# Kernel tuning notes

Measured on AMD Instinct MI355X. Metric: run time of the kernel, lower is better.

The kernel has to match this reference:

```python
import jax, jax.numpy as jnp
import numpy as np
from jax import lax

B, S, K = 256, 2048, 16
E, KE, NI = 20, 17, 30


def crf_nll(emissions, mask, tags, transitions, start_transitions, end_transitions):
    """Mean negative log-likelihood of a linear-chain CRF (pytorch-crf/bert4torch math)."""
    dt = emissions.dtype
    maskf = mask.astype(dt)
    # ---- numerator: score of gold path ----
    em_tag = jnp.take_along_axis(emissions, tags[..., None], axis=2)[..., 0]  # [B,S]
    trans_step = transitions[tags[:, :-1], tags[:, 1:]]                        # [B,S-1]
    num = start_transitions[tags[:, 0]] + em_tag[:, 0]
    num = num + jnp.sum((trans_step + em_tag[:, 1:]) * maskf[:, 1:], axis=1)
    lengths = jnp.sum(mask.astype(jnp.int32), axis=1)                          # [B]
    last_tags = jnp.take_along_axis(tags, (lengths - 1)[:, None], axis=1)[:, 0]
    num = num + end_transitions[last_tags]
    # ---- denominator: log partition via forward algorithm (scan over time) ----
    alpha0 = start_transitions[None, :] + emissions[:, 0]                      # [B,K]

    def step(alpha, xs):
        em_t, m_t = xs                                                         # [B,K], [B]
        nxt = jax.nn.logsumexp(alpha[:, :, None] + transitions[None] + em_t[:, None, :], axis=1)
        alpha = jnp.where(m_t[:, None], nxt, alpha)
        return alpha, None

    alpha, _ = lax.scan(step, alpha0,
                        (emissions[:, 1:].swapaxes(0, 1), mask[:, 1:].swapaxes(0, 1)))
    logZ = jax.nn.logsumexp(alpha + end_transitions[None, :], axis=1)          # [B]
    return jnp.mean(logZ - num)


def cross_entropy_mean(logits, labels):
    logp = jax.nn.log_softmax(logits, axis=-1)
    nll = -jnp.take_along_axis(logp, labels[:, None], axis=1)[:, 0]
    return jnp.mean(nll)


def cross_entropy_ignore0(logits, labels):
    logp = jax.nn.log_softmax(logits, axis=-1)
    nll = -jnp.take_along_axis(logp, labels[:, None], axis=1)[:, 0]
    valid = (labels != 0).astype(logits.dtype)
    return jnp.sum(nll * valid) / jnp.maximum(jnp.sum(valid), 1.0)


def setup_inputs() -> dict:
    key = jax.random.key(0)
    ks = jax.random.split(key, 10)
    emission_score = jax.random.normal(ks[0], (B, S, K), dtype=jnp.float32)
    lengths = jax.random.randint(ks[1], (B,), S // 2, S + 1)
    attention_mask = jnp.arange(S)[None, :] < lengths[:, None]                 # bool [B,S]
    entity_logit = jax.random.normal(ks[2], (B, E, KE), dtype=jnp.float32)
    intent_logit = jax.random.normal(ks[3], (B, NI), dtype=jnp.float32)
    seq_labels = jax.random.randint(ks[4], (B, S), 0, K)
    entity_labels = jax.random.randint(ks[5], (B, E), 0, KE)
    intent_labels = jax.random.randint(ks[6], (B,), 0, NI)
    transitions = jax.random.normal(ks[7], (K, K), dtype=jnp.float32) * 0.1
    start_transitions = jax.random.normal(ks[8], (K,), dtype=jnp.float32) * 0.1
    end_transitions = jax.random.normal(ks[9], (K,), dtype=jnp.float32) * 0.1
    return {"emission_score": emission_score, "attention_mask": attention_mask,
            "entity_logit": entity_logit, "intent_logit": intent_logit,
            "seq_labels": seq_labels, "entity_labels": entity_labels,
            "intent_labels": intent_labels, "transitions": transitions,
            "start_transitions": start_transitions, "end_transitions": end_transitions}


def reference(emission_score, attention_mask, entity_logit, intent_logit,
              seq_labels, entity_labels, intent_labels,
              transitions, start_transitions, end_transitions):
    loss_i = cross_entropy_mean(intent_logit, intent_labels)
    loss_e1 = crf_nll(emission_score, attention_mask, seq_labels,
                      transitions, start_transitions, end_transitions)
    loss_e2 = cross_entropy_ignore0(entity_logit.reshape(-1, entity_logit.shape[-1]),
                                    entity_labels.reshape(-1))
    loss = (loss_e1 + loss_e2 + loss_i) / 3.0
    return (loss, loss_e1, loss_e2, loss_i)
```

## Files before the change

### kernel.cpp

```cpp
#include <hip/hip_runtime.h>
#include <hip/hip_bf16.h>

constexpr int B  = 256, S = 2048, K = 16;
constexpr int E  = 20, KE = 17, NI = 30;
constexpr int C  = 32;
constexpr int L  = S / C;

typedef float    f4 __attribute__((ext_vector_type(4)));
typedef short    s4 __attribute__((ext_vector_type(4)));
typedef unsigned u2 __attribute__((ext_vector_type(2)));

__device__ inline unsigned pk2_trunc(float a, float b) {
  return __builtin_amdgcn_perm(__float_as_uint(b), __float_as_uint(a),
                               0x07060302u);
}

#if __has_builtin(__builtin_amdgcn_mfma_f32_16x16x16bf16_1k)
__device__ inline f4 mfma16(s4 a, s4 b, f4 c) {
  return __builtin_amdgcn_mfma_f32_16x16x16bf16_1k(a, b, c, 0, 0, 0);
}
#else
__device__ inline f4 mfma16(s4 a, s4 b, f4 c) {
  f4 d;
  asm volatile("s_nop 1\n\t"
               "v_mfma_f32_16x16x16_bf16 %0, %1, %2, %3\n\t"
               "s_nop 7\n\ts_nop 7"
               : "=&v"(d) : "v"(a), "v"(b), "v"(c));
  return d;
}
#endif

__global__ __launch_bounds__(1024, 4) void k_fused(
    const float* __restrict__ em,
    const float* __restrict__ trans,
    const int* __restrict__ tags,
    const int* __restrict__ mask,
    const float* __restrict__ startT,
    const float* __restrict__ endT,
    const float* __restrict__ intent_logit,
    const int* __restrict__ intent_labels,
    const float* __restrict__ entity_logit,
    const int* __restrict__ entity_labels,
    float* __restrict__ rowCrf,
    float* __restrict__ rowInt,
    float* __restrict__ rowE2,
    float* __restrict__ rowCnt) {
  __shared__ float tl[256];
  __shared__ alignas(16) float Ml[C * 256];
  __shared__ int   sigl[C];
  __shared__ float numl[16];
  __shared__ int   lenl[16];

  int tid = threadIdx.x;
  if (tid < 256) tl[tid] = trans[tid];
  __syncthreads();

  int w = tid >> 6, lane = tid & 63;
  int b  = blockIdx.x;
  int cA = w;
  int cB = 31 - w;
  int g = lane >> 4, j0 = lane & 15;

  float et0 = __expf(tl[(4 * g + 0) * 16 + j0]);
  float et1 = __expf(tl[(4 * g + 1) * 16 + j0]);
  float et2 = __expf(tl[(4 * g + 2) * 16 + j0]);
  float et3 = __expf(tl[(4 * g + 3) * 16 + j0]);

  int tloA = 1 + cA * L;
  int tloB = 1 + cB * L;
  int WA = min(L, S - tloA);
  int WB = min(L, S - tloB);
  const int* mrow = mask + b * S;
  bool mvA = (lane < WA) && (mrow[tloA + lane] != 0);
  bool mvB = (lane < WB) && (mrow[tloB + lane] != 0);
  int nA = __popcll(__ballot(mvA));
  int nB = __popcll(__ballot(mvB));

  const int* trow = tags + b * S;
  int ttA = tloA + min(lane, WA - 1);
  int ttB = tloB + min(lane, WB - 1);
  int tacA = trow[ttA], tapA = trow[ttA - 1];
  int tacB = trow[ttB], tapB = trow[ttB - 1];
  float numc = 0.f;
  if (lane < nA)
    numc += tl[tapA * 16 + tacA] + em[((size_t)b * S + ttA) * 16 + tacA];
  if (lane < nB)
    numc += tl[tapB * 16 + tacB] + em[((size_t)b * S + ttB) * 16 + tacB];
#pragma unroll
  for (int o = 1; o < 64; o <<= 1) numc += __shfl_xor(numc, o);

  f4 accA, accB;
  accA.x = accB.x = (4 * g + 0 == j0) ? 1.f : 0.f;
  accA.y = accB.y = (4 * g + 1 == j0) ? 1.f : 0.f;
  accA.z = accB.z = (4 * g + 2 == j0) ? 1.f : 0.f;
  accA.w = accB.w = (4 * g + 3 == j0) ? 1.f : 0.f;
  int sigA = 0, sigB = 0;
  const f4 zero4 = {0.f, 0.f, 0.f, 0.f};

  const float* empA = em + ((size_t)b * S + tloA) * 16 + j0;
  const float* empB = em + ((size_t)b * S + tloB) * 16 + j0;

  float curA[8], nxtA[8], curB[8], nxtB[8];
#pragma unroll
  for (int u = 0; u < 8; ++u) { curA[u] = empA[16 * u]; curB[u] = empB[16 * u]; }

#define STEP_A(u_)                                                      \
  {                                                                     \
    float ee = __expf(curA[u_]);                                        \
    unsigned a01 = pk2_trunc(et0 * ee, et1 * ee);                       \
    unsigned a23 = pk2_trunc(et2 * ee, et3 * ee);                       \
    unsigned b01 = pk2_trunc(accA.x, accA.y);                           \
    unsigned b23 = pk2_trunc(accA.z, accA.w);                           \
    s4 Af = __builtin_bit_cast(s4, (u2){a01, a23});                     \
    s4 Bf = __builtin_bit_cast(s4, (u2){b01, b23});                     \
    accA = mfma16(Af, Bf, zero4);                                       \
  }
#define STEP_B(u_)                                                      \
  {                                                                     \
    float ee = __expf(curB[u_]);                                        \
    unsigned a01 = pk2_trunc(et0 * ee, et1 * ee);                       \
    unsigned a23 = pk2_trunc(et2 * ee, et3 * ee);                       \
    unsigned b01 = pk2_trunc(accB.x, accB.y);                           \
    unsigned b23 = pk2_trunc(accB.z, accB.w);                           \
    s4 Af = __builtin_bit_cast(s4, (u2){a01, a23});                     \
    s4 Bf = __builtin_bit_cast(s4, (u2){b01, b23});                     \
    accB = mfma16(Af, Bf, zero4);                                       \
  }
#define RESCALE_A                                                       \
  {                                                                     \
    unsigned fb = __builtin_amdgcn_readfirstlane(__float_as_uint(accA.x));\
    int e = (int)((fb >> 23) & 0xffu) - 127;                            \
    e = max(min(e, 126), -126);                                         \
    float sc = __uint_as_float((unsigned)(127 - e) << 23);              \
    accA.x *= sc; accA.y *= sc; accA.z *= sc; accA.w *= sc;             \
    sigA += e;                                                          \
  }
#define RESCALE_B                                                       \
  {                                                                     \
    unsigned fb = __builtin_amdgcn_readfirstlane(__float_as_uint(accB.x));\
    int e = (int)((fb >> 23) & 0xffu) - 127;                            \
    e = max(min(e, 126), -126);                                         \
    float sc = __uint_as_float((unsigned)(127 - e) << 23);              \
    accB.x *= sc; accB.y *= sc; accB.z *= sc; accB.w *= sc;             \
    sigB += e;                                                          \
  }

  int s = 0;
  for (; s + 8 <= nB; s += 8) {
#pragma unroll
    for (int u = 0; u < 8; ++u) {
      nxtA[u] = empA[16 * min(s + 8 + u, WA - 1)];
      nxtB[u] = empB[16 * min(s + 8 + u, WB - 1)];
    }
#pragma unroll
    for (int u = 0; u < 8; ++u) { STEP_A(u) STEP_B(u) }
    RESCALE_A RESCALE_B
#pragma unroll
    for (int u = 0; u < 8; ++u) { curA[u] = nxtA[u]; curB[u] = nxtB[u]; }
  }
  if (s < nB) {
    int m = nB - s;
#pragma unroll
    for (int u = 0; u < 8; ++u)
      if (u < m) STEP_B(u)
    RESCALE_B
  }
  for (; s + 8 <= nA; s += 8) {
#pragma unroll
    for (int u = 0; u < 8; ++u) nxtA[u] = empA[16 * min(s + 8 + u, WA - 1)];
#pragma unroll
    for (int u = 0; u < 8; ++u) STEP_A(u)
    RESCALE_A
#pragma unroll
    for (int u = 0; u < 8; ++u) curA[u] = nxtA[u];
  }
  if (s < nA) {
    int m = nA - s;
#pragma unroll
    for (int u = 0; u < 8; ++u)
      if (u < m) STEP_A(u)
    RESCALE_A
  }
#undef STEP_A
#undef STEP_B
#undef RESCALE_A
#undef RESCALE_B

  int base = (j0 >> 2) * 64 + 16 * g + (j0 & 3);
  float* moA = &Ml[cA * 256];
  moA[base + 0]  = accA.x;
  moA[base + 4]  = accA.y;
  moA[base + 8]  = accA.z;
  moA[base + 12] = accA.w;
  float* moB = &Ml[cB * 256];
  moB[base + 0]  = accB.x;
  moB[base + 4]  = accB.y;
  moB[base + 8]  = accB.z;
  moB[base + 12] = accB.w;
  if (lane == 0) {
    sigl[cA] = sigA;
    sigl[cB] = sigB;
    numl[w]  = numc;
    lenl[w]  = nA + nB + (cA == 0 ? 1 : 0);
  }
  __syncthreads();

  if (w == 0) {
    int l = lane, jb = l & 15, ib = l >> 4;

    float numtot = (l < 16) ? numl[l] : 0.f;
    int   lentot = (l < 16) ? lenl[l] : 0;
#pragma unroll
    for (int o = 1; o < 16; o <<= 1) {
      numtot += __shfl_xor(numtot, o);
      lentot += __shfl_xor(lentot, o);
    }

    const float* erow = em + (size_t)b * S * 16;
    float a0 = startT[jb] + erow[jb];
    float m0 = a0;
#pragma unroll
    for (int o = 1; o < 16; o <<= 1) m0 = fmaxf(m0, __shfl_xor(m0, o));
    float v = __expf(a0 - m0);
    float total = m0;
    int tg0 = tags[(size_t)b * S];
    float num0 = __shfl(a0, tg0);

    int sv = (l < C) ? sigl[l] : 0;
    const f4* mptr = (const f4*)Ml;
    f4 p0 = mptr[0 * 64 + l], p1 = mptr[1 * 64 + l];
    f4 p2 = mptr[2 * 64 + l], p3 = mptr[3 * 64 + l];

#define PROC(p_, c_)                                                         \
    {                                                                        \
      float v0 = __shfl(v, 4 * ib + 0), v1 = __shfl(v, 4 * ib + 1);          \
      float v2 = __shfl(v, 4 * ib + 2), v3 = __shfl(v, 4 * ib + 3);          \
      float sacc = v0 * p_.x + v1 * p_.y + v2 * p_.z + v3 * p_.w;            \
      sacc += __shfl_xor(sacc, 16); sacc += __shfl_xor(sacc, 32);            \
      float mx = sacc;                                                       \
      for (int o = 1; o < 16; o <<= 1) mx = fmaxf(mx, __shfl_xor(mx, o));    \
      int e = (int)((__float_as_uint(mx) >> 23) & 0xffu) - 127;              \
      e = max(min(e, 126), -126);                                            \
      float sc = __uint_as_float((unsigned)(127 - e) << 23);                 \
      v = sacc * sc;                                                         \
      total += (float)(__shfl(sv, (c_)) + e) * 0.6931471805599453f;          \
    }

    for (int cc = 0; cc < C; cc += 4) {
      PROC(p0, cc + 0) if (cc + 4 < C) p0 = mptr[(cc + 4) * 64 + l];
      PROC(p1, cc + 1) if (cc + 4 < C) p1 = mptr[(cc + 5) * 64 + l];
      PROC(p2, cc + 2) if (cc + 4 < C) p2 = mptr[(cc + 6) * 64 + l];
      PROC(p3, cc + 3) if (cc + 4 < C) p3 = mptr[(cc + 7) * 64 + l];
    }
#undef PROC

    float term = v * __expf(endT[jb]);
#pragma unroll
    for (int o = 1; o < 16; o <<= 1) term += __shfl_xor(term, o);
    if (l == 0) {
      float logZ = __logf(term) + total;
      float numb = numtot + num0 + endT[tags[(size_t)b * S + lentot - 1]];
      rowCrf[b] = logZ - numb;
    }
  } else if (w == 1) {
    int l = lane;
    const float* row = intent_logit + b * NI;
    float x = (l < NI) ? row[l] : -1e30f;
    float mi = x;
#pragma unroll
    for (int o = 1; o < 64; o <<= 1) mi = fmaxf(mi, __shfl_xor(mi, o));
    float se = (l < NI) ? __expf(x - mi) : 0.f;
#pragma unroll
    for (int o = 1; o < 64; o <<= 1) se += __shfl_xor(se, o);

    float nll2 = 0.f, cnt2 = 0.f;
    if (l < E) {
      const float* er = entity_logit + (size_t)(b * E + l) * KE;
      float me = -1e30f;
      for (int k = 0; k < KE; ++k) me = fmaxf(me, er[k]);
      float ss = 0.f;
      for (int k = 0; k < KE; ++k) ss += __expf(er[k] - me);
      int lb = entity_labels[b * E + l];
      if (lb != 0) { nll2 = -(er[lb] - me - __logf(ss)); cnt2 = 1.f; }
    }
#pragma unroll
    for (int o = 1; o < 64; o <<= 1) {
      nll2 += __shfl_xor(nll2, o);
      cnt2 += __shfl_xor(cnt2, o);
    }
    if (l == 0) {
      int lab = intent_labels[b];
      rowInt[b] = -(row[lab] - mi - __logf(se));
      rowE2[b]  = nll2;
      rowCnt[b] = cnt2;
    }
  }
}

__global__ __launch_bounds__(256) void k_final(const float* __restrict__ rowCrf,
                                               const float* __restrict__ rowInt,
                                               const float* __restrict__ rowE2,
                                               const float* __restrict__ rowCnt,
                                               float* __restrict__ out) {
  int tid = threadIdx.x;
  float s0 = rowCrf[tid], s1 = rowInt[tid], s2 = rowE2[tid], s3 = rowCnt[tid];
  __shared__ float r[4][4];
#pragma unroll
  for (int o = 32; o; o >>= 1) {
    s0 += __shfl_down(s0, o); s1 += __shfl_down(s1, o);
    s2 += __shfl_down(s2, o); s3 += __shfl_down(s3, o);
  }
  if ((tid & 63) == 0) {
    r[tid >> 6][0] = s0; r[tid >> 6][1] = s1;
    r[tid >> 6][2] = s2; r[tid >> 6][3] = s3;
  }
  __syncthreads();
  if (tid == 0) {
    float crf = r[0][0] + r[1][0] + r[2][0] + r[3][0];
    float it  = r[0][1] + r[1][1] + r[2][1] + r[3][1];
    float e2  = r[0][2] + r[1][2] + r[2][2] + r[3][2];
    float cn  = r[0][3] + r[1][3] + r[2][3] + r[3][3];
    float le1 = crf / (float)B;
    float li  = it  / (float)B;
    float le2 = e2 / fmaxf(cn, 1.f);
    out[0] = (le1 + le2 + li) / 3.f;
    out[1] = le1;
    out[2] = le2;
    out[3] = li;
  }
}

extern "C" void kernel_launch(void* const* d_in, const int* in_sizes, int n_in,
                              void* d_out, int out_size, void* d_ws, size_t ws_size,
                              hipStream_t stream) {
  const float* em            = (const float*)d_in[0];
  const int*   mask          = (const int*)  d_in[1];
  const float* entity_logit  = (const float*)d_in[2];
  const float* intent_logit  = (const float*)d_in[3];
  const int*   seq_labels    = (const int*)  d_in[4];
  const int*   entity_labels = (const int*)  d_in[5];
  const int*   intent_labels = (const int*)  d_in[6];
  const float* trans         = (const float*)d_in[7];
  const float* startT        = (const float*)d_in[8];
  const float* endT          = (const float*)d_in[9];
  float* out = (float*)d_out;

  char* ws = (char*)d_ws;
  float* rowCrf = (float*)ws;
  float* rowInt = (float*)(ws + 1024);
  float* rowE2  = (float*)(ws + 2048);
  float* rowCnt = (float*)(ws + 3072);

  k_fused<<<B, 1024, 0, stream>>>(em, trans, seq_labels, mask, startT, endT,
                                  intent_logit, intent_labels,
                                  entity_logit, entity_labels,
                                  rowCrf, rowInt, rowE2, rowCnt);
  k_final<<<1, 256, 0, stream>>>(rowCrf, rowInt, rowE2, rowCnt, out);
}
```

Before: 32.48 us.

## Stage emission chunks into LDS via async global_load_lds with graded waitcnts

Each wave now issues all of its emission loads for both time chunks up front, using global_load_lds into a per-wave LDS staging buffer, plus a few register loads for the tail steps. The scan is then fully unrolled in groups of eight steps, and each group waits only on the vmcnt needed for its data. The aim is to hide global-memory latency behind the serial MFMA recurrence, replacing the register double-buffer and its loop overhead. In exchange it adds roughly 120KB of LDS and relies on hand-counted vmcnt values. It also drops the width guards for chunk A, on the assumption that those chunks are always full.

```diff
diff --git a/kernel.cpp b/kernel.cpp
--- a/kernel.cpp
+++ b/kernel.cpp
@@ -29,6 +29,8 @@
   return d;
 }
 #endif
+
+#define SWAIT(s_) asm volatile("s_waitcnt vmcnt(" s_ ")" ::: "memory")
 
 __global__ __launch_bounds__(1024, 4) void k_fused(
     const float* __restrict__ em,
@@ -46,6 +48,7 @@
     float* __restrict__ rowE2,
     float* __restrict__ rowCnt) {
   __shared__ float tl[256];
+  __shared__ float stage[16 * 2 * 960];
   __shared__ alignas(16) float Ml[C * 256];
   __shared__ int   sigl[C];
   __shared__ float numl[16];
@@ -59,25 +62,24 @@
   int b  = blockIdx.x;
   int cA = w;
   int cB = 31 - w;
-  int g = lane >> 4, j0 = lane & 15;
-
-  float et0 = __expf(tl[(4 * g + 0) * 16 + j0]);
-  float et1 = __expf(tl[(4 * g + 1) * 16 + j0]);
-  float et2 = __expf(tl[(4 * g + 2) * 16 + j0]);
-  float et3 = __expf(tl[(4 * g + 3) * 16 + j0]);
+  int g4 = lane >> 4, j0 = lane & 15;
+
+  float et0 = __expf(tl[(4 * g4 + 0) * 16 + j0]);
+  float et1 = __expf(tl[(4 * g4 + 1) * 16 + j0]);
+  float et2 = __expf(tl[(4 * g4 + 2) * 16 + j0]);
+  float et3 = __expf(tl[(4 * g4 + 3) * 16 + j0]);
 
   int tloA = 1 + cA * L;
   int tloB = 1 + cB * L;
-  int WA = min(L, S - tloA);
   int WB = min(L, S - tloB);
   const int* mrow = mask + b * S;
-  bool mvA = (lane < WA) && (mrow[tloA + lane] != 0);
+  bool mvA = (mrow[tloA + lane] != 0);
   bool mvB = (lane < WB) && (mrow[tloB + lane] != 0);
   int nA = __popcll(__ballot(mvA));
   int nB = __popcll(__ballot(mvB));
 
   const int* trow = tags + b * S;
-  int ttA = tloA + min(lane, WA - 1);
+  int ttA = tloA + lane;
   int ttB = tloB + min(lane, WB - 1);
   int tacA = trow[ttA], tapA = trow[ttA - 1];
   int tacB = trow[ttB], tapB = trow[ttB - 1];
@@ -90,23 +92,38 @@
   for (int o = 1; o < 64; o <<= 1) numc += __shfl_xor(numc, o);
 
   f4 accA, accB;
-  accA.x = accB.x = (4 * g + 0 == j0) ? 1.f : 0.f;
-  accA.y = accB.y = (4 * g + 1 == j0) ? 1.f : 0.f;
-  accA.z = accB.z = (4 * g + 2 == j0) ? 1.f : 0.f;
-  accA.w = accB.w = (4 * g + 3 == j0) ? 1.f : 0.f;
+  accA.x = accB.x = (4 * g4 + 0 == j0) ? 1.f : 0.f;
+  accA.y = accB.y = (4 * g4 + 1 == j0) ? 1.f : 0.f;
+  accA.z = accB.z = (4 * g4 + 2 == j0) ? 1.f : 0.f;
+  accA.w = accB.w = (4 * g4 + 3 == j0) ? 1.f : 0.f;
   int sigA = 0, sigB = 0;
   const f4 zero4 = {0.f, 0.f, 0.f, 0.f};
 
-  const float* empA = em + ((size_t)b * S + tloA) * 16 + j0;
-  const float* empB = em + ((size_t)b * S + tloB) * 16 + j0;
-
-  float curA[8], nxtA[8], curB[8], nxtB[8];
-#pragma unroll
-  for (int u = 0; u < 8; ++u) { curA[u] = empA[16 * u]; curB[u] = empB[16 * u]; }
-
-#define STEP_A(u_)                                                      \
-  {                                                                     \
-    float ee = __expf(curA[u_]);                                        \
+  const float* gA = em + ((size_t)b * S + tloA) * 16;
+  const float* gB = em + ((size_t)b * S + tloB) * 16;
+  float* lAw = &stage[(2 * w + 0) * 960];
+  float* lBw = &stage[(2 * w + 1) * 960];
+
+  asm volatile("" ::: "memory");
+#pragma unroll
+  for (int k = 0; k < 15; ++k) {
+    __builtin_amdgcn_global_load_lds(gA + 64 * k + lane, lAw + 64 * k, 4, 0, 0);
+    __builtin_amdgcn_global_load_lds(gB + 64 * k + lane, lBw + 64 * k, 4, 0, 0);
+  }
+  asm volatile("" ::: "memory");
+  float rA[4], rB[4];
+#pragma unroll
+  for (int u = 0; u < 4; ++u) {
+    rA[u] = gA[16 * (60 + u) + j0];
+    rB[u] = gB[16 * min(60 + u, WB - 1) + j0];
+  }
+
+  const float* sA = lAw + j0;
+  const float* sB = lBw + j0;
+
+#define STEP_A_L(st_)                                                   \
+  {                                                                     \
+    float ee = __expf(sA[(st_) * 16]);                                  \
     unsigned a01 = pk2_trunc(et0 * ee, et1 * ee);                       \
     unsigned a23 = pk2_trunc(et2 * ee, et3 * ee);                       \
     unsigned b01 = pk2_trunc(accA.x, accA.y);                           \
@@ -115,9 +132,9 @@
     s4 Bf = __builtin_bit_cast(s4, (u2){b01, b23});                     \
     accA = mfma16(Af, Bf, zero4);                                       \
   }
-#define STEP_B(u_)                                                      \
-  {                                                                     \
-    float ee = __expf(curB[u_]);                                        \
+#define STEP_B_L(st_)                                                   \
+  {                                                                     \
+    float ee = __expf(sB[(st_) * 16]);                                  \
     unsigned a01 = pk2_trunc(et0 * ee, et1 * ee);                       \
     unsigned a23 = pk2_trunc(et2 * ee, et3 * ee);                       \
     unsigned b01 = pk2_trunc(accB.x, accB.y);                           \
@@ -126,6 +143,28 @@
     s4 Bf = __builtin_bit_cast(s4, (u2){b01, b23});                     \
     accB = mfma16(Af, Bf, zero4);                                       \
   }
+#define STEP_A_R(u_)                                                    \
+  {                                                                     \
+    float ee = __expf(rA[u_]);                                          \
+    unsigned a01 = pk2_trunc(et0 * ee, et1 * ee);                       \
+    unsigned a23 = pk2_trunc(et2 * ee, et3 * ee);                       \
+    unsigned b01 = pk2_trunc(accA.x, accA.y);                           \
+    unsigned b23 = pk2_trunc(accA.z, accA.w);                           \
+    s4 Af = __builtin_bit_cast(s4, (u2){a01, a23});                     \
+    s4 Bf = __builtin_bit_cast(s4, (u2){b01, b23});                     \
+    accA = mfma16(Af, Bf, zero4);                                       \
+  }
+#define STEP_B_R(u_)                                                    \
+  {                                                                     \
+    float ee = __expf(rB[u_]);                                          \
+    unsigned a01 = pk2_trunc(et0 * ee, et1 * ee);                       \
+    unsigned a23 = pk2_trunc(et2 * ee, et3 * ee);                       \
+    unsigned b01 = pk2_trunc(accB.x, accB.y);                           \
+    unsigned b23 = pk2_trunc(accB.z, accB.w);                           \
+    s4 Af = __builtin_bit_cast(s4, (u2){a01, a23});                     \
+    s4 Bf = __builtin_bit_cast(s4, (u2){b01, b23});                     \
+    accB = mfma16(Af, Bf, zero4);                                       \
+  }
 #define RESCALE_A                                                       \
   {                                                                     \
     unsigned fb = __builtin_amdgcn_readfirstlane(__float_as_uint(accA.x));\
@@ -145,48 +184,64 @@
     sigB += e;                                                          \
   }
 
-  int s = 0;
-  for (; s + 8 <= nB; s += 8) {
-#pragma unroll
-    for (int u = 0; u < 8; ++u) {
-      nxtA[u] = empA[16 * min(s + 8 + u, WA - 1)];
-      nxtB[u] = empB[16 * min(s + 8 + u, WB - 1)];
-    }
-#pragma unroll
-    for (int u = 0; u < 8; ++u) { STEP_A(u) STEP_B(u) }
-    RESCALE_A RESCALE_B
-#pragma unroll
-    for (int u = 0; u < 8; ++u) { curA[u] = nxtA[u]; curB[u] = nxtB[u]; }
-  }
-  if (s < nB) {
-    int m = nB - s;
-#pragma unroll
-    for (int u = 0; u < 8; ++u)
-      if (u < m) STEP_B(u)
-    RESCALE_B
-  }
-  for (; s + 8 <= nA; s += 8) {
-#pragma unroll
-    for (int u = 0; u < 8; ++u) nxtA[u] = empA[16 * min(s + 8 + u, WA - 1)];
-#pragma unroll
-    for (int u = 0; u < 8; ++u) STEP_A(u)
+#define AB8(g_)                                                         \
+  STEP_A_L(8*g_+0) STEP_B_L(8*g_+0) STEP_A_L(8*g_+1) STEP_B_L(8*g_+1)   \
+  STEP_A_L(8*g_+2) STEP_B_L(8*g_+2) STEP_A_L(8*g_+3) STEP_B_L(8*g_+3)   \
+  STEP_A_L(8*g_+4) STEP_B_L(8*g_+4) STEP_A_L(8*g_+5) STEP_B_L(8*g_+5)   \
+  STEP_A_L(8*g_+6) STEP_B_L(8*g_+6) STEP_A_L(8*g_+7) STEP_B_L(8*g_+7)
+#define A8(g_)                                                          \
+  STEP_A_L(8*g_+0) STEP_A_L(8*g_+1) STEP_A_L(8*g_+2) STEP_A_L(8*g_+3)   \
+  STEP_A_L(8*g_+4) STEP_A_L(8*g_+5) STEP_A_L(8*g_+6) STEP_A_L(8*g_+7)
+#define GROUP(g_, NW_)                                                  \
+  {                                                                     \
+    SWAIT(NW_);                                                         \
+    if (nB >= 8 * g_ + 8) {                                             \
+      AB8(g_) RESCALE_A RESCALE_B                                       \
+    } else {                                                            \
+      A8(g_) RESCALE_A                                                  \
+      int mB_ = nB - 8 * g_;                                            \
+      if (mB_ > 0) {                                                    \
+        if (mB_ > 0) STEP_B_L(8*g_+0) if (mB_ > 1) STEP_B_L(8*g_+1)     \
+        if (mB_ > 2) STEP_B_L(8*g_+2) if (mB_ > 3) STEP_B_L(8*g_+3)     \
+        if (mB_ > 4) STEP_B_L(8*g_+4) if (mB_ > 5) STEP_B_L(8*g_+5)     \
+        if (mB_ > 6) STEP_B_L(8*g_+6) if (mB_ > 7) STEP_B_L(8*g_+7)     \
+        RESCALE_B                                                       \
+      }                                                                 \
+    }                                                                   \
+  }
+
+  GROUP(0, "34") GROUP(1, "30") GROUP(2, "26") GROUP(3, "22")
+  GROUP(4, "18") GROUP(5, "14") GROUP(6, "10")
+
+  {
+    SWAIT("0");
+    int mA = nA - 56;
+    STEP_A_L(56) STEP_A_L(57) STEP_A_L(58) STEP_A_L(59)
+    if (mA > 4) STEP_A_R(0)
+    if (mA > 5) STEP_A_R(1)
+    if (mA > 6) STEP_A_R(2)
+    if (mA > 7) STEP_A_R(3)
     RESCALE_A
-#pragma unroll
-    for (int u = 0; u < 8; ++u) curA[u] = nxtA[u];
-  }
-  if (s < nA) {
-    int m = nA - s;
-#pragma unroll
-    for (int u = 0; u < 8; ++u)
-      if (u < m) STEP_A(u)
-    RESCALE_A
-  }
-#undef STEP_A
-#undef STEP_B
+    int mB = nB - 56;
+    if (mB > 0) {
+      if (mB > 0) STEP_B_L(56) if (mB > 1) STEP_B_L(57)
+      if (mB > 2) STEP_B_L(58) if (mB > 3) STEP_B_L(59)
+      if (mB > 4) STEP_B_R(0) if (mB > 5) STEP_B_R(1)
+      if (mB > 6) STEP_B_R(2)
+      RESCALE_B
+    }
+  }
+#undef GROUP
+#undef AB8
+#undef A8
+#undef STEP_A_L
+#undef STEP_B_L
+#undef STEP_A_R
+#undef STEP_B_R
 #undef RESCALE_A
 #undef RESCALE_B
 
-  int base = (j0 >> 2) * 64 + 16 * g + (j0 & 3);
+  int base = (j0 >> 2) * 64 + 16 * g4 + (j0 & 3);
   float* moA = &Ml[cA * 256];
   moA[base + 0]  = accA.x;
   moA[base + 4]  = accA.y;
```

Result: no change. 32.58 us (+0.3%).

## Split each chunk's transfer-matrix chain into four parallel sub-chains staged in LDS

Applied to the files above, without the earlier changes.

Each wave's two 64-step chunks are now reduced as four independent 16-step chains each: one forward chain and three chains built from transposed transitions. These are combined at the end with three extra MFMA products. Emission exponentials are computed once and staged in a 128 KB LDS buffer, which replaces the per-step global loads and prefetch registers. The aim is to cut the serial MFMA dependency depth per wave from 64 to about 19, so more independent MFMAs can be in flight. The cost is far more LDS, which limits occupancy to one block per CU, plus more bf16 truncation in the combining products.

```diff
diff --git a/kernel.cpp b/kernel.cpp
--- a/kernel.cpp
+++ b/kernel.cpp
@@ -46,7 +46,7 @@
     float* __restrict__ rowE2,
     float* __restrict__ rowCnt) {
   __shared__ float tl[256];
-  __shared__ alignas(16) float Ml[C * 256];
+  __shared__ alignas(16) float stage[16 * 2048];
   __shared__ int   sigl[C];
   __shared__ float numl[16];
   __shared__ int   lenl[16];
@@ -59,144 +59,145 @@
   int b  = blockIdx.x;
   int cA = w;
   int cB = 31 - w;
-  int g = lane >> 4, j0 = lane & 15;
-
-  float et0 = __expf(tl[(4 * g + 0) * 16 + j0]);
-  float et1 = __expf(tl[(4 * g + 1) * 16 + j0]);
-  float et2 = __expf(tl[(4 * g + 2) * 16 + j0]);
-  float et3 = __expf(tl[(4 * g + 3) * 16 + j0]);
+  int g4 = lane >> 4, j0 = lane & 15;
 
   int tloA = 1 + cA * L;
   int tloB = 1 + cB * L;
-  int WA = min(L, S - tloA);
   int WB = min(L, S - tloB);
+
+  float* stA = stage + w * 2048;
+  float* stB = stA + 1024;
+
+  {
+    int tAs = tloA + lane;
+    int tBs = tloB + min(lane, WB - 1);
+    const float* gAs = em + ((size_t)b * S + tAs) * 16;
+    const float* gBs = em + ((size_t)b * S + tBs) * 16;
+#pragma unroll
+    for (int q = 0; q < 4; ++q) {
+      f4 va = *(const f4*)(gAs + 4 * q);
+      f4 vb = *(const f4*)(gBs + 4 * q);
+      f4 ea, eb;
+      ea.x = __expf(va.x); ea.y = __expf(va.y);
+      ea.z = __expf(va.z); ea.w = __expf(va.w);
+      eb.x = __expf(vb.x); eb.y = __expf(vb.y);
+      eb.z = __expf(vb.z); eb.w = __expf(vb.w);
+      *(f4*)(stA + lane * 16 + 4 * q) = ea;
+      *(f4*)(stB + lane * 16 + 4 * q) = eb;
+    }
+  }
+
   const int* mrow = mask + b * S;
-  bool mvA = (lane < WA) && (mrow[tloA + lane] != 0);
+  bool mvA = (mrow[tloA + lane] != 0);
   bool mvB = (lane < WB) && (mrow[tloB + lane] != 0);
-  int nA = __popcll(__ballot(mvA));
-  int nB = __popcll(__ballot(mvB));
 
   const int* trow = tags + b * S;
-  int ttA = tloA + min(lane, WA - 1);
+  int ttA = tloA + lane;
   int ttB = tloB + min(lane, WB - 1);
   int tacA = trow[ttA], tapA = trow[ttA - 1];
   int tacB = trow[ttB], tapB = trow[ttB - 1];
-  float numc = 0.f;
-  if (lane < nA)
-    numc += tl[tapA * 16 + tacA] + em[((size_t)b * S + ttA) * 16 + tacA];
-  if (lane < nB)
-    numc += tl[tapB * 16 + tacB] + em[((size_t)b * S + ttB) * 16 + tacB];
-#pragma unroll
-  for (int o = 1; o < 64; o <<= 1) numc += __shfl_xor(numc, o);
-
-  f4 accA, accB;
-  accA.x = accB.x = (4 * g + 0 == j0) ? 1.f : 0.f;
-  accA.y = accB.y = (4 * g + 1 == j0) ? 1.f : 0.f;
-  accA.z = accB.z = (4 * g + 2 == j0) ? 1.f : 0.f;
-  accA.w = accB.w = (4 * g + 3 == j0) ? 1.f : 0.f;
+  float gAv = em[((size_t)b * S + ttA) * 16 + tacA];
+  float gBv = em[((size_t)b * S + ttB) * 16 + tacB];
+
+  int nA = __popcll(__ballot(mvA));
+  int nB = __popcll(__ballot(mvB));
+
+  float etF0 = __expf(tl[(4 * g4 + 0) * 16 + j0]);
+  float etF1 = __expf(tl[(4 * g4 + 1) * 16 + j0]);
+  float etF2 = __expf(tl[(4 * g4 + 2) * 16 + j0]);
+  float etF3 = __expf(tl[(4 * g4 + 3) * 16 + j0]);
+  float etT0 = __expf(tl[j0 * 16 + 4 * g4 + 0]);
+  float etT1 = __expf(tl[j0 * 16 + 4 * g4 + 1]);
+  float etT2 = __expf(tl[j0 * 16 + 4 * g4 + 2]);
+  float etT3 = __expf(tl[j0 * 16 + 4 * g4 + 3]);
+
+  f4 ID;
+  ID.x = (4 * g4 + 0 == j0) ? 1.f : 0.f;
+  ID.y = (4 * g4 + 1 == j0) ? 1.f : 0.f;
+  ID.z = (4 * g4 + 2 == j0) ? 1.f : 0.f;
+  ID.w = (4 * g4 + 3 == j0) ? 1.f : 0.f;
+  f4 Y0A = ID, X1A = ID, X2A = ID, X3A = ID;
+  f4 Y0B = ID, X1B = ID, X2B = ID, X3B = ID;
   int sigA = 0, sigB = 0;
   const f4 zero4 = {0.f, 0.f, 0.f, 0.f};
 
-  const float* empA = em + ((size_t)b * S + tloA) * 16 + j0;
-  const float* empB = em + ((size_t)b * S + tloB) * 16 + j0;
-
-  float curA[8], nxtA[8], curB[8], nxtB[8];
-#pragma unroll
-  for (int u = 0; u < 8; ++u) { curA[u] = empA[16 * u]; curB[u] = empB[16 * u]; }
-
-#define STEP_A(u_)                                                      \
-  {                                                                     \
-    float ee = __expf(curA[u_]);                                        \
-    unsigned a01 = pk2_trunc(et0 * ee, et1 * ee);                       \
-    unsigned a23 = pk2_trunc(et2 * ee, et3 * ee);                       \
-    unsigned b01 = pk2_trunc(accA.x, accA.y);                           \
-    unsigned b23 = pk2_trunc(accA.z, accA.w);                           \
-    s4 Af = __builtin_bit_cast(s4, (u2){a01, a23});                     \
-    s4 Bf = __builtin_bit_cast(s4, (u2){b01, b23});                     \
-    accA = mfma16(Af, Bf, zero4);                                       \
-  }
-#define STEP_B(u_)                                                      \
-  {                                                                     \
-    float ee = __expf(curB[u_]);                                        \
-    unsigned a01 = pk2_trunc(et0 * ee, et1 * ee);                       \
-    unsigned a23 = pk2_trunc(et2 * ee, et3 * ee);                       \
-    unsigned b01 = pk2_trunc(accB.x, accB.y);                           \
-    unsigned b23 = pk2_trunc(accB.z, accB.w);                           \
-    s4 Af = __builtin_bit_cast(s4, (u2){a01, a23});                     \
-    s4 Bf = __builtin_bit_cast(s4, (u2){b01, b23});                     \
-    accB = mfma16(Af, Bf, zero4);                                       \
-  }
-#define RESCALE_A                                                       \
-  {                                                                     \
-    unsigned fb = __builtin_amdgcn_readfirstlane(__float_as_uint(accA.x));\
+#define STEPF(st_, row_, ACC_)                                          \
+  { float ee = (st_)[(row_) * 16 + j0];                                 \
+    unsigned a01 = pk2_trunc(etF0 * ee, etF1 * ee);                     \
+    unsigned a23 = pk2_trunc(etF2 * ee, etF3 * ee);                     \
+    unsigned b01 = pk2_trunc(ACC_.x, ACC_.y);                           \
+    unsigned b23 = pk2_trunc(ACC_.z, ACC_.w);                           \
+    ACC_ = mfma16(__builtin_bit_cast(s4, (u2){a01, a23}),               \
+                  __builtin_bit_cast(s4, (u2){b01, b23}), zero4); }
+#define STEPB(st_, row_, ACC_)                                          \
+  { f4 ev = *(const f4*)((st_) + (row_) * 16 + 4 * g4);                 \
+    unsigned a01 = pk2_trunc(etT0 * ev.x, etT1 * ev.y);                 \
+    unsigned a23 = pk2_trunc(etT2 * ev.z, etT3 * ev.w);                 \
+    unsigned b01 = pk2_trunc(ACC_.x, ACC_.y);                           \
+    unsigned b23 = pk2_trunc(ACC_.z, ACC_.w);                           \
+    ACC_ = mfma16(__builtin_bit_cast(s4, (u2){a01, a23}),               \
+                  __builtin_bit_cast(s4, (u2){b01, b23}), zero4); }
+#define RES(ACC_, SIG_)                                                 \
+  { unsigned fb = __builtin_amdgcn_readfirstlane(__float_as_uint(ACC_.x));\
     int e = (int)((fb >> 23) & 0xffu) - 127;                            \
     e = max(min(e, 126), -126);                                         \
     float sc = __uint_as_float((unsigned)(127 - e) << 23);              \
-    accA.x *= sc; accA.y *= sc; accA.z *= sc; accA.w *= sc;             \
-    sigA += e;                                                          \
-  }
-#define RESCALE_B                                                       \
-  {                                                                     \
-    unsigned fb = __builtin_amdgcn_readfirstlane(__float_as_uint(accB.x));\
-    int e = (int)((fb >> 23) & 0xffu) - 127;                            \
-    e = max(min(e, 126), -126);                                         \
-    float sc = __uint_as_float((unsigned)(127 - e) << 23);              \
-    accB.x *= sc; accB.y *= sc; accB.z *= sc; accB.w *= sc;             \
-    sigB += e;                                                          \
-  }
-
-  int s = 0;
-  for (; s + 8 <= nB; s += 8) {
-#pragma unroll
-    for (int u = 0; u < 8; ++u) {
-      nxtA[u] = empA[16 * min(s + 8 + u, WA - 1)];
-      nxtB[u] = empB[16 * min(s + 8 + u, WB - 1)];
-    }
-#pragma unroll
-    for (int u = 0; u < 8; ++u) { STEP_A(u) STEP_B(u) }
-    RESCALE_A RESCALE_B
-#pragma unroll
-    for (int u = 0; u < 8; ++u) { curA[u] = nxtA[u]; curB[u] = nxtB[u]; }
-  }
-  if (s < nB) {
-    int m = nB - s;
-#pragma unroll
-    for (int u = 0; u < 8; ++u)
-      if (u < m) STEP_B(u)
-    RESCALE_B
-  }
-  for (; s + 8 <= nA; s += 8) {
-#pragma unroll
-    for (int u = 0; u < 8; ++u) nxtA[u] = empA[16 * min(s + 8 + u, WA - 1)];
-#pragma unroll
-    for (int u = 0; u < 8; ++u) STEP_A(u)
-    RESCALE_A
-#pragma unroll
-    for (int u = 0; u < 8; ++u) curA[u] = nxtA[u];
-  }
-  if (s < nA) {
-    int m = nA - s;
-#pragma unroll
-    for (int u = 0; u < 8; ++u)
-      if (u < m) STEP_A(u)
-    RESCALE_A
-  }
-#undef STEP_A
-#undef STEP_B
-#undef RESCALE_A
-#undef RESCALE_B
-
-  int base = (j0 >> 2) * 64 + 16 * g + (j0 & 3);
+    ACC_.x *= sc; ACC_.y *= sc; ACC_.z *= sc; ACC_.w *= sc;             \
+    SIG_ += e; }
+#define OPC(U_, V_, OUT_)                                               \
+  { unsigned ua = pk2_trunc(U_.x, U_.y), ub = pk2_trunc(U_.z, U_.w);    \
+    unsigned va = pk2_trunc(V_.x, V_.y), vb = pk2_trunc(V_.z, V_.w);    \
+    OUT_ = mfma16(__builtin_bit_cast(s4, (u2){ua, ub}),                 \
+                  __builtin_bit_cast(s4, (u2){va, vb}), zero4); }
+
+#pragma unroll
+  for (int u = 0; u < 16; ++u) {
+    STEPF(stA, u, Y0A)
+    if (u < nB) STEPF(stB, u, Y0B)
+    STEPB(stA, 31 - u, X1A)
+    if (31 - u < nB) STEPB(stB, 31 - u, X1B)
+    STEPB(stA, 47 - u, X2A)
+    if (47 - u < nB) STEPB(stB, 47 - u, X2B)
+    if (63 - u < nA) STEPB(stA, 63 - u, X3A)
+    if (63 - u < nB) STEPB(stB, 63 - u, X3B)
+    if (u == 7 || u == 15) {
+      RES(Y0A, sigA) RES(X1A, sigA) RES(X2A, sigA) RES(X3A, sigA)
+      RES(Y0B, sigB) RES(X1B, sigB) RES(X2B, sigB) RES(X3B, sigB)
+    }
+  }
+
+  f4 oA, pA, MA, oB, pB, MB;
+  OPC(X1A, Y0A, oA) RES(oA, sigA)
+  OPC(X2A, oA,  pA) RES(pA, sigA)
+  OPC(X3A, pA,  MA) RES(MA, sigA)
+  OPC(X1B, Y0B, oB) RES(oB, sigB)
+  OPC(X2B, oB,  pB) RES(pB, sigB)
+  OPC(X3B, pB,  MB) RES(MB, sigB)
+#undef STEPF
+#undef STEPB
+#undef RES
+#undef OPC
+
+  float numc = 0.f;
+  if (lane < nA) numc += tl[tapA * 16 + tacA] + gAv;
+  if (lane < nB) numc += tl[tapB * 16 + tacB] + gBv;
+#pragma unroll
+  for (int o = 1; o < 64; o <<= 1) numc += __shfl_xor(numc, o);
+
+  __syncthreads();
+
+  float* Ml = stage;
+  int base = (j0 >> 2) * 64 + 16 * g4 + (j0 & 3);
   float* moA = &Ml[cA * 256];
-  moA[base + 0]  = accA.x;
-  moA[base + 4]  = accA.y;
-  moA[base + 8]  = accA.z;
-  moA[base + 12] = accA.w;
+  moA[base + 0]  = MA.x;
+  moA[base + 4]  = MA.y;
+  moA[base + 8]  = MA.z;
+  moA[base + 12] = MA.w;
   float* moB = &Ml[cB * 256];
-  moB[base + 0]  = accB.x;
-  moB[base + 4]  = accB.y;
-  moB[base + 8]  = accB.z;
-  moB[base + 12] = accB.w;
+  moB[base + 0]  = MB.x;
+  moB[base + 4]  = MB.y;
+  moB[base + 8]  = MB.z;
+  moB[base + 12] = MB.w;
   if (lane == 0) {
     sigl[cA] = sigA;
     sigl[cB] = sigB;
@@ -217,17 +218,17 @@
     }
 
     const float* erow = em + (size_t)b * S * 16;
-    float a0 = startT[jb] + erow[jb];
-    float m0 = a0;
+    float a0v = startT[jb] + erow[jb];
+    float m0 = a0v;
 #pragma unroll
     for (int o = 1; o < 16; o <<= 1) m0 = fmaxf(m0, __shfl_xor(m0, o));
-    float v = __expf(a0 - m0);
+    float v = __expf(a0v - m0);
     float total = m0;
     int tg0 = tags[(size_t)b * S];
-    float num0 = __shfl(a0, tg0);
+    float num0 = __shfl(a0v, tg0);
 
     int sv = (l < C) ? sigl[l] : 0;
-    const f4* mptr = (const f4*)Ml;
+    const f4* mptr = (const f4*)stage;
     f4 p0 = mptr[0 * 64 + l], p1 = mptr[1 * 64 + l];
     f4 p2 = mptr[2 * 64 + l], p3 = mptr[3 * 64 + l];
 
```

Result: no change. 32.07 us (-1.3%).
